# Kernel optimization log

Measured on AMD Instinct MI355X. Metric: run time of the kernel, lower is better.

The kernel has to match this reference:

```python
import jax, jax.numpy as jnp
import numpy as np

M = 8      # quantization steps
K = 256    # codewords per step
D = 128    # vector dim
H = 256    # hidden dim of residual MLP
S = M - 1  # number of neural steps (steps 1..M-1)
L = 2      # residual blocks per step
BEAM = 16  # beam width (cfg.B)
A = 8      # substep shortlist size (n_codes)
B = 2048   # batch


def setup_inputs() -> dict:
    key = jax.random.key(0)
    ks = jax.random.split(key, 16)
    sc = 0.05
    f32 = jnp.float32
    return {
        "x": jax.random.normal(ks[0], (B, D), f32),
        "codebook": jax.random.normal(ks[1], (M, K, D), f32) * sc,
        "codebook_rq": jax.random.normal(ks[2], (S, K, D), f32) * sc,
        "W_in": jax.random.normal(ks[3], (S, D, H), f32) * (D ** -0.5),
        "b_in": jnp.zeros((S, H), f32),
        "W_cat": jax.random.normal(ks[4], (S, H + D, H), f32) * ((H + D) ** -0.5),
        "b_cat": jnp.zeros((S, H), f32),
        "W1": jax.random.normal(ks[5], (S, L, H, H), f32) * (H ** -0.5),
        "b1": jnp.zeros((S, L, H), f32),
        "W2": jax.random.normal(ks[6], (S, L, H, H), f32) * (H ** -0.5),
        "b2": jnp.zeros((S, L, H), f32),
        "W_out": jax.random.normal(ks[7], (S, H, D), f32) * (H ** -0.5),
        "b_out": jnp.zeros((S, D), f32),
    }


def _approx_dist(q, cb):
    # approx squared L2 dist, dropping the query norm: ||c||^2 - 2 q.c
    # q: (..., D), cb: (K, D) -> (..., K)
    return jnp.sum(cb * cb, axis=-1) - 2.0 * q @ cb.T


def reference(x, codebook, codebook_rq, W_in, b_in, W_cat, b_cat,
              W1, b1, W2, b2, W_out, b_out):
    # --- step 0: plain codebook lookup, keep top-BEAM candidates ---
    d0 = _approx_dist(x, codebook[0])                  # (B, K)
    _, codes0 = jax.lax.top_k(-d0, BEAM)               # (B, BEAM) smallest dists
    xhat = codebook[0][codes0]                          # (B, BEAM, D)
    codes_list = [codes0]

    for s in range(S):
        i_step = s + 1
        F_in = xhat.shape[1]
        F_out = BEAM if i_step < M - 1 else 1

        # substep pre-filter: shortlist A codes per beam element
        xt = x[:, None, :] - xhat                      # (B, F, D)
        d = _approx_dist(xt, codebook_rq[s])           # (B, F, K)
        _, top_c = jax.lax.top_k(-d, A)                # (B, F, A)
        cw = codebook[i_step][top_c]                   # gather: (B, F, A, D)
        cw_res = cw

        # residual MLP conditioned on current xhat
        h = cw @ W_in[s] + b_in[s]                     # (B, F, A, H)
        xb = jnp.broadcast_to(xhat[:, :, None, :], cw.shape)
        h = jnp.concatenate([h, xb], axis=-1) @ W_cat[s] + b_cat[s]
        for l in range(L):
            h = h + jax.nn.relu(h @ W1[s, l] + b1[s, l]) @ W2[s, l] + b2[s, l]
        cw = h @ W_out[s] + b_out[s] + cw_res          # res_codeword_coeff = 1.0

        # re-score flattened beam*shortlist candidates and prune to F_out
        cand = (cw + xhat[:, :, None, :]).reshape(B, F_in * A, D)
        d2 = jnp.sum(cand * cand, axis=-1) - 2.0 * jnp.einsum('bd,bkd->bk', x, cand)
        _, idx = jax.lax.top_k(-d2, F_out)             # (B, F_out)

        parent = idx // A                               # == repeat_interleave+gather
        codes_list = [jnp.take_along_axis(c, parent, axis=-1) for c in codes_list]
        codes_list.append(jnp.take_along_axis(top_c.reshape(B, F_in * A), idx, axis=-1))
        xhat = jnp.take_along_axis(cand, idx[:, :, None], axis=1)  # (B, F_out, D)

    codes_MB = jnp.stack([c[:, 0] for c in codes_list])  # (M, B), final beam = 1
    return codes_MB, xhat[:, 0, :]
```

## Files before the change

### kernel.cpp

```cpp
#include <hip/hip_runtime.h>
#include <float.h>

#define BB    2048
#define DD    128
#define KK    256
#define HH    256
#define MM    8
#define SS    7
#define BEAMW 16
#define AA    8
#define WM    64

typedef _Float16 f16x8 __attribute__((ext_vector_type(8)));
typedef float    f32x4 __attribute__((ext_vector_type(4)));

#define HSWZ(row, m) (((row) << 5) + ((((m) + ((((row) >> 3)) << 2))) & 31))

__device__ __forceinline__ int hoff(int m, int j) {
  return m * 256 + ((((j >> 3) ^ (m & 7)) << 3) | (j & 7));
}

__global__ __launch_bounds__(64) void step0_kernel(
    const float* __restrict__ x, const float* __restrict__ cb,
    float* __restrict__ xhat, int* __restrict__ codes)
{
  int b = blockIdx.x, l = threadIdx.x;
  __shared__ float xs[DD];
  xs[l]      = x[b * DD + l];
  xs[l + 64] = x[b * DD + 64 + l];
  __syncthreads();
  float dist[4];
#pragma unroll
  for (int q = 0; q < 4; ++q) {
    const float* row = cb + (size_t)(q * 64 + l) * DD;
    float dot = 0.f, nrm = 0.f;
#pragma unroll 8
    for (int d = 0; d < DD; d += 4) {
      float4 c = *(const float4*)(row + d);
      dot += c.x * xs[d] + c.y * xs[d + 1] + c.z * xs[d + 2] + c.w * xs[d + 3];
      nrm += c.x * c.x + c.y * c.y + c.z * c.z + c.w * c.w;
    }
    dist[q] = nrm - 2.f * dot;
  }
  for (int it = 0; it < BEAMW; ++it) {
    float bv = dist[0]; int bi = l;
#pragma unroll
    for (int q = 1; q < 4; ++q) {
      if (dist[q] < bv) { bv = dist[q]; bi = q * 64 + l; }
    }
#pragma unroll
    for (int mmk = 1; mmk < 64; mmk <<= 1) {
      float ov = __shfl_xor(bv, mmk);
      int   oi = __shfl_xor(bi, mmk);
      if (ov < bv || (ov == bv && oi < bi)) { bv = ov; bi = oi; }
    }
    const float* crow = cb + (size_t)bi * DD;
    float2 v = *(const float2*)(crow + l * 2);
    *(float2*)(xhat + (size_t)(b * BEAMW + it) * DD + l * 2) = v;
    if (l == 0) codes[(b * BEAMW + it) * MM] = bi;
    if (l == (bi & 63)) dist[bi >> 6] = FLT_MAX;
  }
}

__global__ __launch_bounds__(128) void rqprep_kernel(
    const float* __restrict__ rq, float* __restrict__ rqT, float* __restrict__ rqn)
{
  int k = blockIdx.x, d = threadIdx.x;
  float v = rq[k * DD + d];
  rqT[d * KK + k] = v;
  float p = v * v;
#pragma unroll
  for (int mmk = 1; mmk < 64; mmk <<= 1) p += __shfl_xor(p, mmk);
  __shared__ float ps[2];
  if ((d & 63) == 0) ps[d >> 6] = p;
  __syncthreads();
  if (d == 0) rqn[k] = ps[0] + ps[1];
}

__global__ __launch_bounds__(256) void codeterm_kernel(
    const float* __restrict__ cbstep, const float* __restrict__ Win,
    const float* __restrict__ bin, const float* __restrict__ Wcat,
    const float* __restrict__ bcat, float* __restrict__ ct)
{
  int k = blockIdx.x, j = threadIdx.x;
  __shared__ float crow[DD];
  __shared__ float h1[HH];
  if (j < DD) crow[j] = cbstep[k * DD + j];
  __syncthreads();
  float a = bin[j];
  for (int d = 0; d < DD; ++d) a += crow[d] * Win[d * HH + j];
  h1[j] = a;
  __syncthreads();
  float c = bcat[j];
  for (int t = 0; t < HH; ++t) c += h1[t] * Wcat[t * HH + j];
  ct[k * HH + j] = c;
}

__global__ __launch_bounds__(256) void wpack_kernel(
    const float* __restrict__ W1s, const float* __restrict__ W2s,
    const float* __restrict__ Wouts, const float* __restrict__ Wcat2s,
    _Float16* __restrict__ wAh, _Float16* __restrict__ wAl,
    _Float16* __restrict__ woh, _Float16* __restrict__ wol,
    _Float16* __restrict__ wch, _Float16* __restrict__ wcl)
{
  int t = blockIdx.x * 256 + threadIdx.x;
  const float* src; _Float16 *dh, *dl;
  int N, r;
  if (t < 32768) {
    int mi = t >> 13; r = t & 8191;
    src = (mi & 1 ? W2s : W1s) + (size_t)(mi >> 1) * HH * HH;
    dh = wAh + (size_t)mi * 65536; dl = wAl + (size_t)mi * 65536;
    N = 256;
  } else if (t < 36864) {
    r = t - 32768; src = Wouts; dh = woh; dl = wol; N = 128;
  } else {
    r = t - 36864; src = Wcat2s; dh = wch; dl = wcl; N = 256;
  }
  int l = r & 63;
  int nct = N >> 4;
  int c = (r >> 6) & (nct - 1);
  int q = r / (64 * nct);
  int k0 = q * 32 + (l >> 4) * 8;
  int col = c * 16 + (l & 15);
  size_t fo = (size_t)r * 8;
#pragma unroll
  for (int j = 0; j < 8; ++j) {
    float v = src[(size_t)(k0 + j) * N + col];
    _Float16 hi = (_Float16)v;
    dh[fo + j] = hi;
    dl[fo + j] = (_Float16)((v - (float)hi) * 2048.0f);
  }
}

__global__ __launch_bounds__(256) void xterm_kernel(
    const float* __restrict__ xhat,
    const _Float16* __restrict__ wch, const _Float16* __restrict__ wcl,
    float* __restrict__ xtg)
{
  int tid = threadIdx.x;
  int l = tid & 63, w = tid >> 6;
  int lg = l >> 4, lr = l & 15;
  int r0 = blockIdx.x * 16;
  const f32x4 z4 = {0.f, 0.f, 0.f, 0.f};
  f32x4 a1[4], a2[4];
#pragma unroll
  for (int c = 0; c < 4; ++c) { a1[c] = z4; a2[c] = z4; }
  for (int q = 0; q < 4; ++q) {
    const float* ap = xhat + (size_t)(r0 + lr) * DD + q * 32 + lg * 8;
    float4 f0 = *(const float4*)ap;
    float4 f1 = *(const float4*)(ap + 4);
    float fv[8] = {f0.x, f0.y, f0.z, f0.w, f1.x, f1.y, f1.z, f1.w};
    f16x8 Ah, Al;
#pragma unroll
    for (int j = 0; j < 8; ++j) {
      _Float16 hi = (_Float16)fv[j];
      Ah[j] = hi;
      Al[j] = (_Float16)((fv[j] - (float)hi) * 2048.0f);
    }
#pragma unroll
    for (int c = 0; c < 4; ++c) {
      size_t boff = ((size_t)(q * 16 + w * 4 + c) * 64 + l) * 8;
      f16x8 Bh = *(const f16x8*)&wch[boff];
      f16x8 Bl = *(const f16x8*)&wcl[boff];
      a1[c] = __builtin_amdgcn_mfma_f32_16x16x32_f16(Ah, Bh, a1[c], 0, 0, 0);
      a2[c] = __builtin_amdgcn_mfma_f32_16x16x32_f16(Al, Bh, a2[c], 0, 0, 0);
      a2[c] = __builtin_amdgcn_mfma_f32_16x16x32_f16(Ah, Bl, a2[c], 0, 0, 0);
    }
  }
#pragma unroll
  for (int c = 0; c < 4; ++c) {
    int col = (w * 4 + c) * 16 + lr;
#pragma unroll
    for (int r = 0; r < 4; ++r) {
      int row = r0 + lg * 4 + r;
      xtg[(size_t)row * 256 + col] = a1[c][r] + a2[c][r] * (1.0f / 2048.0f);
    }
  }
}

__global__ __launch_bounds__(256) void prefilter_kernel(
    const float* __restrict__ x, const float* __restrict__ xhat,
    const float* __restrict__ rqT, const float* __restrict__ rqn,
    int* __restrict__ topc)
{
  __shared__ float xtT[DD * 32];
  __shared__ float distb[32 * KK];
  int tid = threadIdx.x;
  int bf0 = blockIdx.x * 32;
  for (int i = 0; i < 16; ++i) {
    int idx = tid + i * 256;
    int d = idx >> 5, r = idx & 31;
    int bf = bf0 + r;
    xtT[HSWZ(d, r)] = x[(bf >> 4) * DD + d] - xhat[(size_t)bf * DD + d];
  }
  __syncthreads();
  int jb = tid & 31, mb = tid >> 5;
  float acc[4][8];
#pragma unroll
  for (int i = 0; i < 4; ++i)
#pragma unroll
    for (int jj = 0; jj < 8; ++jj) acc[i][jj] = 0.f;
  for (int d = 0; d < DD; ++d) {
    float4 hv = *(float4*)&xtT[HSWZ(d, mb * 4)];
    float4 w0 = *(const float4*)&rqT[d * KK + jb * 8];
    float4 w1 = *(const float4*)&rqT[d * KK + jb * 8 + 4];
    float hvv[4] = {hv.x, hv.y, hv.z, hv.w};
    float wv[8]  = {w0.x, w0.y, w0.z, w0.w, w1.x, w1.y, w1.z, w1.w};
#pragma unroll
    for (int i = 0; i < 4; ++i)
#pragma unroll
      for (int jj = 0; jj < 8; ++jj) acc[i][jj] += hvv[i] * wv[jj];
  }
#pragma unroll
  for (int i = 0; i < 4; ++i) {
    int r = mb * 4 + i;
#pragma unroll
    for (int jj = 0; jj < 8; ++jj) {
      int k = jb * 8 + jj;
      distb[r * KK + k] = rqn[k] - 2.f * acc[i][jj];
    }
  }
  __syncthreads();
  int wv2 = tid >> 6, lane = tid & 63;
  for (int rr = 0; rr < 8; ++rr) {
    int r = wv2 * 8 + rr;
    float v[4];
#pragma unroll
    for (int q = 0; q < 4; ++q) v[q] = distb[r * KK + lane + q * 64];
    int bfr = bf0 + r;
    for (int it = 0; it < AA; ++it) {
      float bv = v[0]; int bi = lane;
#pragma unroll
      for (int q = 1; q < 4; ++q) {
        if (v[q] < bv) { bv = v[q]; bi = q * 64 + lane; }
      }
#pragma unroll
      for (int mmk = 1; mmk < 64; mmk <<= 1) {
        float ov = __shfl_xor(bv, mmk);
        int   oi = __shfl_xor(bi, mmk);
        if (ov < bv || (ov == bv && oi < bi)) { bv = ov; bi = oi; }
      }
      if (lane == (bi & 63)) v[bi >> 6] = FLT_MAX;
      if (lane == 0) topc[bfr * AA + it] = bi;
    }
  }
}

__global__ __launch_bounds__(1024, 4) void mlp_kernel(
    const float* __restrict__ x, const float* __restrict__ xhat,
    const int* __restrict__ topc, const float* __restrict__ ct,
    const float* __restrict__ cbstep, const float* __restrict__ xtg,
    const _Float16* __restrict__ wAh, const _Float16* __restrict__ wAl,
    const _Float16* __restrict__ woh, const _Float16* __restrict__ wol,
    const float* __restrict__ b1a, const float* __restrict__ b2a,
    const float* __restrict__ bout,
    float* __restrict__ cand, float* __restrict__ d2g)
{
  __shared__ _Float16 hhi[WM * 256], hlo[WM * 256];
  __shared__ float xs[DD];
  __shared__ float pd2[WM][8];
  __shared__ int   cl[WM];

  int tid = threadIdx.x;
  int l = tid & 63, w = tid >> 6;
  int lg = l >> 4, lr = l & 15;
  int bf0 = blockIdx.x * 8;
  int b = bf0 >> 4;
  const f32x4 z4 = {0.f, 0.f, 0.f, 0.f};

  if (tid < WM) cl[tid] = topc[bf0 * AA + tid];
  if (tid < DD) xs[tid] = x[b * DD + tid];
  __syncthreads();

  for (int i = 0; i < 16; ++i) {
    int e = tid + i * 1024;
    int m = e >> 8, j = e & 255;
    float v = ct[cl[m] * HH + j] + xtg[(size_t)(bf0 + (m >> 3)) * 256 + j];
    _Float16 hi = (_Float16)v;
    int off = hoff(m, j);
    hhi[off] = hi;
    hlo[off] = (_Float16)((v - (float)hi) * 2048.0f);
  }
  __syncthreads();

  int j0 = w * 16 + lr;

  for (int lay = 0; lay < 2; ++lay) {
    const _Float16* W1h = wAh + (size_t)(lay * 2 + 0) * 65536;
    const _Float16* W1l = wAl + (size_t)(lay * 2 + 0) * 65536;
    const _Float16* W2h = wAh + (size_t)(lay * 2 + 1) * 65536;
    const _Float16* W2l = wAl + (size_t)(lay * 2 + 1) * 65536;
    const float* bb1 = b1a + lay * HH;
    const float* bb2 = b2a + lay * HH;

    f32x4 a1[4], a2[4];
#pragma unroll
    for (int rt = 0; rt < 4; ++rt) { a1[rt] = z4; a2[rt] = z4; }
    for (int q = 0; q < 8; ++q) {
      size_t boff = ((size_t)(q * 16 + w) * 64 + l) * 8;
      f16x8 Bh = *(const f16x8*)&W1h[boff];
      f16x8 Bl = *(const f16x8*)&W1l[boff];
#pragma unroll
      for (int rt = 0; rt < 4; ++rt) {
        int arow = rt * 16 + lr;
        int aoff = arow * 256 + (((q * 4 + lg) ^ (arow & 7)) << 3);
        f16x8 Ah = *(f16x8*)&hhi[aoff];
        f16x8 Al = *(f16x8*)&hlo[aoff];
        a1[rt] = __builtin_amdgcn_mfma_f32_16x16x32_f16(Ah, Bh, a1[rt], 0, 0, 0);
        a2[rt] = __builtin_amdgcn_mfma_f32_16x16x32_f16(Al, Bh, a2[rt], 0, 0, 0);
        a2[rt] = __builtin_amdgcn_mfma_f32_16x16x32_f16(Ah, Bl, a2[rt], 0, 0, 0);
      }
    }
    {
      float bj = bb1[j0];
#pragma unroll
      for (int rt = 0; rt < 4; ++rt)
#pragma unroll
        for (int r = 0; r < 4; ++r) {
          int m = rt * 16 + lg * 4 + r;
          float u = fmaxf(a1[rt][r] + a2[rt][r] * (1.0f / 2048.0f) + bj, 0.f);
          int off = hoff(m, j0);
          float res = (float)hhi[off] + (float)hlo[off] * (1.0f / 2048.0f);
          a1[rt][r] = u;
          a2[rt][r] = res;
        }
    }
    __syncthreads();
#pragma unroll
    for (int rt = 0; rt < 4; ++rt)
#pragma unroll
      for (int r = 0; r < 4; ++r) {
        int m = rt * 16 + lg * 4 + r;
        float v = a1[rt][r];
        _Float16 hi = (_Float16)v;
        int off = hoff(m, j0);
        hhi[off] = hi;
        hlo[off] = (_Float16)((v - (float)hi) * 2048.0f);
      }
    __syncthreads();

#pragma unroll
    for (int rt = 0; rt < 4; ++rt) {
      a1[rt] = a2[rt];
      a2[rt] = z4;
    }
    for (int q = 0; q < 8; ++q) {
      size_t boff = ((size_t)(q * 16 + w) * 64 + l) * 8;
      f16x8 Bh = *(const f16x8*)&W2h[boff];
      f16x8 Bl = *(const f16x8*)&W2l[boff];
#pragma unroll
      for (int rt = 0; rt < 4; ++rt) {
        int arow = rt * 16 + lr;
        int aoff = arow * 256 + (((q * 4 + lg) ^ (arow & 7)) << 3);
        f16x8 Ah = *(f16x8*)&hhi[aoff];
        f16x8 Al = *(f16x8*)&hlo[aoff];
        a1[rt] = __builtin_amdgcn_mfma_f32_16x16x32_f16(Ah, Bh, a1[rt], 0, 0, 0);
        a2[rt] = __builtin_amdgcn_mfma_f32_16x16x32_f16(Al, Bh, a2[rt], 0, 0, 0);
        a2[rt] = __builtin_amdgcn_mfma_f32_16x16x32_f16(Ah, Bl, a2[rt], 0, 0, 0);
      }
    }
    {
      float bj = bb2[j0];
#pragma unroll
      for (int rt = 0; rt < 4; ++rt)
#pragma unroll
        for (int r = 0; r < 4; ++r)
          a1[rt][r] += a2[rt][r] * (1.0f / 2048.0f) + bj;
    }
    __syncthreads();
#pragma unroll
    for (int rt = 0; rt < 4; ++rt)
#pragma unroll
      for (int r = 0; r < 4; ++r) {
        int m = rt * 16 + lg * 4 + r;
        float v = a1[rt][r];
        _Float16 hi = (_Float16)v;
        int off = hoff(m, j0);
        hhi[off] = hi;
        hlo[off] = (_Float16)((v - (float)hi) * 2048.0f);
      }
    __syncthreads();
  }

  int c8 = w & 7, mh = w >> 3;
  f32x4 o1[2], o2[2];
  o1[0] = z4; o1[1] = z4; o2[0] = z4; o2[1] = z4;
  for (int q = 0; q < 8; ++q) {
    size_t boff = ((size_t)(q * 8 + c8) * 64 + l) * 8;
    f16x8 Bh = *(const f16x8*)&woh[boff];
    f16x8 Bl = *(const f16x8*)&wol[boff];
#pragma unroll
    for (int rr = 0; rr < 2; ++rr) {
      int arow = (mh * 2 + rr) * 16 + lr;
      int aoff = arow * 256 + (((q * 4 + lg) ^ (arow & 7)) << 3);
      f16x8 Ah = *(f16x8*)&hhi[aoff];
      f16x8 Al = *(f16x8*)&hlo[aoff];
      o1[rr] = __builtin_amdgcn_mfma_f32_16x16x32_f16(Ah, Bh, o1[rr], 0, 0, 0);
      o2[rr] = __builtin_amdgcn_mfma_f32_16x16x32_f16(Al, Bh, o2[rr], 0, 0, 0);
      o2[rr] = __builtin_amdgcn_mfma_f32_16x16x32_f16(Ah, Bl, o2[rr], 0, 0, 0);
    }
  }
  int ci0 = (blockIdx.x & 1) * WM;
  int d = c8 * 16 + lr;
  float bo = bout[d];
  float xsd = xs[d];
#pragma unroll
  for (int rr = 0; rr < 2; ++rr) {
    int rt = mh * 2 + rr;
    float p[4];
#pragma unroll
    for (int r = 0; r < 4; ++r) {
      int m = rt * 16 + lg * 4 + r;
      float v = o1[rr][r] + o2[rr][r] * (1.0f / 2048.0f) + bo
              + cbstep[(size_t)cl[m] * DD + d]
              + xhat[(size_t)(bf0 + (m >> 3)) * DD + d];
      cand[((size_t)(b * 128 + ci0 + m)) * DD + d] = v;
      p[r] = v * (v - 2.f * xsd);
    }
#pragma unroll
    for (int mk = 1; mk < 16; mk <<= 1) {
#pragma unroll
      for (int r = 0; r < 4; ++r) p[r] += __shfl_xor(p[r], mk);
    }
    if (lr == 0) {
#pragma unroll
      for (int r = 0; r < 4; ++r) pd2[rt * 16 + lg * 4 + r][c8] = p[r];
    }
  }
  __syncthreads();
  if (tid < WM) {
    float s = 0.f;
#pragma unroll
    for (int ww = 0; ww < 8; ++ww) s += pd2[tid][ww];
    d2g[b * 128 + ci0 + tid] = s;
  }
}

__global__ __launch_bounds__(64) void topk_update_kernel(
    const float* __restrict__ d2g, const float* __restrict__ cand,
    const int* __restrict__ codes_in, const int* __restrict__ topc,
    float* __restrict__ xhat_out, int* __restrict__ codes_out,
    int fout, int spos)
{
  int b = blockIdx.x, lane = threadIdx.x;
  float v0 = d2g[b * 128 + lane];
  float v1 = d2g[b * 128 + 64 + lane];
  for (int r = 0; r < fout; ++r) {
    float bv = v0; int bi = lane;
    if (v1 < bv) { bv = v1; bi = 64 + lane; }
#pragma unroll
    for (int mmk = 1; mmk < 64; mmk <<= 1) {
      float ov = __shfl_xor(bv, mmk);
      int   oi = __shfl_xor(bi, mmk);
      if (ov < bv || (ov == bv && oi < bi)) { bv = ov; bi = oi; }
    }
    int parent = bi >> 3, a = bi & 7;
    if (lane < MM) {
      int valc = (lane == spos) ? topc[(b * BEAMW + parent) * AA + a]
                                : codes_in[(b * BEAMW + parent) * MM + lane];
      codes_out[(b * BEAMW + r) * MM + lane] = valc;
    }
    const float* src = cand + ((size_t)(b * 128 + bi)) * DD;
    float2 t = *(const float2*)(src + lane * 2);
    *(float2*)(xhat_out + (size_t)(b * BEAMW + r) * DD + lane * 2) = t;
    if (bi < 64) { if (lane == bi) v0 = FLT_MAX; }
    else         { if (lane == bi - 64) v1 = FLT_MAX; }
  }
}

__global__ __launch_bounds__(64) void finalize_kernel(
    const int* __restrict__ codes_fin, const float* __restrict__ xhat_fin,
    float* __restrict__ out)
{
  int b = blockIdx.x, lane = threadIdx.x;
  float2 t = *(const float2*)(xhat_fin + (size_t)(b * BEAMW) * DD + lane * 2);
  *(float2*)(out + (size_t)MM * BB + (size_t)b * DD + lane * 2) = t;
  if (lane < MM) out[lane * BB + b] = (float)codes_fin[(b * BEAMW) * MM + lane];
}

extern "C" void kernel_launch(void* const* d_in, const int* in_sizes, int n_in,
                              void* d_out, int out_size, void* d_ws, size_t ws_size,
                              hipStream_t stream)
{
  (void)in_sizes; (void)n_in; (void)out_size; (void)ws_size;
  const float* x    = (const float*)d_in[0];
  const float* cb   = (const float*)d_in[1];
  const float* rq   = (const float*)d_in[2];
  const float* Win  = (const float*)d_in[3];
  const float* bin  = (const float*)d_in[4];
  const float* Wcat = (const float*)d_in[5];
  const float* bcat = (const float*)d_in[6];
  const float* W1   = (const float*)d_in[7];
  const float* b1   = (const float*)d_in[8];
  const float* W2   = (const float*)d_in[9];
  const float* b2   = (const float*)d_in[10];
  const float* Wout = (const float*)d_in[11];
  const float* bout = (const float*)d_in[12];
  float* out = (float*)d_out;

  char* ws = (char*)d_ws;
  size_t off = 0;
  auto alloc = [&](size_t bytes) -> void* {
    void* p = ws + off;
    off += (bytes + 255) & ~(size_t)255;
    return p;
  };
  float* X0    = (float*)alloc((size_t)BB * BEAMW * DD * 4);
  float* X1    = (float*)alloc((size_t)BB * BEAMW * DD * 4);
  int*   C0    = (int*)  alloc((size_t)BB * BEAMW * MM * 4);
  int*   C1    = (int*)  alloc((size_t)BB * BEAMW * MM * 4);
  int*   tc    = (int*)  alloc((size_t)BB * BEAMW * AA * 4);
  float* rqT   = (float*)alloc((size_t)DD * KK * 4);
  float* rqn   = (float*)alloc((size_t)KK * 4);
  float* ct    = (float*)alloc((size_t)KK * HH * 4);
  float* d2b   = (float*)alloc((size_t)BB * 128 * 4);
  float* candb = (float*)alloc((size_t)BB * 128 * DD * 4);
  float* xtg   = (float*)alloc((size_t)BB * BEAMW * 256 * 4);
  _Float16* wAh = (_Float16*)alloc((size_t)4 * 65536 * 2);
  _Float16* wAl = (_Float16*)alloc((size_t)4 * 65536 * 2);
  _Float16* woh = (_Float16*)alloc((size_t)32768 * 2);
  _Float16* wol = (_Float16*)alloc((size_t)32768 * 2);
  _Float16* wch = (_Float16*)alloc((size_t)32768 * 2);
  _Float16* wcl = (_Float16*)alloc((size_t)32768 * 2);

  step0_kernel<<<BB, 64, 0, stream>>>(x, cb, X0, C0);
  float* Xc = X0; float* Xn = X1;
  int* Cc = C0; int* Cn = C1;
  for (int s = 0; s < SS; ++s) {
    wpack_kernel<<<160, 256, 0, stream>>>(
        W1 + (size_t)s * 2 * HH * HH, W2 + (size_t)s * 2 * HH * HH,
        Wout + (size_t)s * HH * DD,
        Wcat + (size_t)s * 384 * HH + (size_t)256 * HH,
        wAh, wAl, woh, wol, wch, wcl);
    rqprep_kernel<<<KK, DD, 0, stream>>>(rq + (size_t)s * KK * DD, rqT, rqn);
    codeterm_kernel<<<KK, HH, 0, stream>>>(cb + (size_t)(s + 1) * KK * DD,
        Win + (size_t)s * DD * HH, bin + (size_t)s * HH,
        Wcat + (size_t)s * 384 * HH, bcat + (size_t)s * HH, ct);
    prefilter_kernel<<<(BB * BEAMW) / 32, 256, 0, stream>>>(x, Xc, rqT, rqn, tc);
    xterm_kernel<<<(BB * BEAMW) / 16, 256, 0, stream>>>(Xc, wch, wcl, xtg);
    mlp_kernel<<<(BB * BEAMW * AA) / WM, 1024, 0, stream>>>(x, Xc, tc, ct,
        cb + (size_t)(s + 1) * KK * DD, xtg,
        wAh, wAl, woh, wol,
        b1 + (size_t)s * 2 * HH, b2 + (size_t)s * 2 * HH,
        bout + (size_t)s * DD,
        candb, d2b);
    int fo = (s < SS - 1) ? BEAMW : 1;
    topk_update_kernel<<<BB, 64, 0, stream>>>(d2b, candb, Cc, tc, Xn, Cn, fo, s + 1);
    { float* t = Xc; Xc = Xn; Xn = t; }
    { int* t = Cc; Cc = Cn; Cn = t; }
  }
  finalize_kernel<<<BB, 64, 0, stream>>>(Cc, Xc, out);
}
```

Baseline: 4.654 ms.

## Batch per-step weight prep into single launches and keep MLP residual in registers

Weight packing, rq transpose/norm and codeword-term precomputation for all seven steps now run once, up front, in three launches writing per-step buffers, replacing 21 small launches inside the step loop. In the MLP kernel, the residual stream is kept in fp32 registers and the ReLU intermediate goes to separate LDS buffers (uhi/ulo). This drops one barrier plus a full LDS rewrite per half-layer and the hi/lo residual reconstruction. The cost is doubled LDS for the activation tiles (about 128KB per block), which may limit occupancy or fail to fit, plus larger workspace buffers.

```diff
diff --git a/kernel.cpp b/kernel.cpp
--- a/kernel.cpp
+++ b/kernel.cpp
@@ -63,58 +63,70 @@
 }
 
 __global__ __launch_bounds__(128) void rqprep_kernel(
-    const float* __restrict__ rq, float* __restrict__ rqT, float* __restrict__ rqn)
-{
-  int k = blockIdx.x, d = threadIdx.x;
-  float v = rq[k * DD + d];
-  rqT[d * KK + k] = v;
+    const float* __restrict__ rq, float* __restrict__ rqT7, float* __restrict__ rqn7)
+{
+  int s = blockIdx.x >> 8, k = blockIdx.x & 255, d = threadIdx.x;
+  float v = rq[(size_t)s * KK * DD + k * DD + d];
+  rqT7[(size_t)s * DD * KK + d * KK + k] = v;
   float p = v * v;
 #pragma unroll
   for (int mmk = 1; mmk < 64; mmk <<= 1) p += __shfl_xor(p, mmk);
   __shared__ float ps[2];
   if ((d & 63) == 0) ps[d >> 6] = p;
   __syncthreads();
-  if (d == 0) rqn[k] = ps[0] + ps[1];
+  if (d == 0) rqn7[s * KK + k] = ps[0] + ps[1];
 }
 
 __global__ __launch_bounds__(256) void codeterm_kernel(
-    const float* __restrict__ cbstep, const float* __restrict__ Win,
+    const float* __restrict__ cb, const float* __restrict__ Win,
     const float* __restrict__ bin, const float* __restrict__ Wcat,
-    const float* __restrict__ bcat, float* __restrict__ ct)
-{
-  int k = blockIdx.x, j = threadIdx.x;
+    const float* __restrict__ bcat, float* __restrict__ ct7)
+{
+  int s = blockIdx.x >> 8, k = blockIdx.x & 255, j = threadIdx.x;
+  const float* cbstep = cb + (size_t)(s + 1) * KK * DD;
+  const float* WinS   = Win + (size_t)s * DD * HH;
+  const float* WcatS  = Wcat + (size_t)s * 384 * HH;
   __shared__ float crow[DD];
   __shared__ float h1[HH];
   if (j < DD) crow[j] = cbstep[k * DD + j];
   __syncthreads();
-  float a = bin[j];
-  for (int d = 0; d < DD; ++d) a += crow[d] * Win[d * HH + j];
+  float a = bin[s * HH + j];
+  for (int d = 0; d < DD; ++d) a += crow[d] * WinS[d * HH + j];
   h1[j] = a;
   __syncthreads();
-  float c = bcat[j];
-  for (int t = 0; t < HH; ++t) c += h1[t] * Wcat[t * HH + j];
-  ct[k * HH + j] = c;
+  float c = bcat[s * HH + j];
+  for (int t = 0; t < HH; ++t) c += h1[t] * WcatS[t * HH + j];
+  ct7[(size_t)s * KK * HH + k * HH + j] = c;
 }
 
 __global__ __launch_bounds__(256) void wpack_kernel(
-    const float* __restrict__ W1s, const float* __restrict__ W2s,
-    const float* __restrict__ Wouts, const float* __restrict__ Wcat2s,
-    _Float16* __restrict__ wAh, _Float16* __restrict__ wAl,
-    _Float16* __restrict__ woh, _Float16* __restrict__ wol,
-    _Float16* __restrict__ wch, _Float16* __restrict__ wcl)
-{
-  int t = blockIdx.x * 256 + threadIdx.x;
+    const float* __restrict__ W1, const float* __restrict__ W2,
+    const float* __restrict__ Wout, const float* __restrict__ Wcat,
+    _Float16* __restrict__ wAh7, _Float16* __restrict__ wAl7,
+    _Float16* __restrict__ woh7, _Float16* __restrict__ wol7,
+    _Float16* __restrict__ wch7, _Float16* __restrict__ wcl7)
+{
+  int tg = blockIdx.x * 256 + threadIdx.x;
+  int s = tg / 40960;
+  int t = tg % 40960;
   const float* src; _Float16 *dh, *dl;
   int N, r;
   if (t < 32768) {
     int mi = t >> 13; r = t & 8191;
-    src = (mi & 1 ? W2s : W1s) + (size_t)(mi >> 1) * HH * HH;
-    dh = wAh + (size_t)mi * 65536; dl = wAl + (size_t)mi * 65536;
+    src = (mi & 1 ? W2 : W1) + (size_t)s * 2 * HH * HH + (size_t)(mi >> 1) * HH * HH;
+    dh = wAh7 + (size_t)s * 262144 + (size_t)mi * 65536;
+    dl = wAl7 + (size_t)s * 262144 + (size_t)mi * 65536;
     N = 256;
   } else if (t < 36864) {
-    r = t - 32768; src = Wouts; dh = woh; dl = wol; N = 128;
+    r = t - 32768;
+    src = Wout + (size_t)s * HH * DD;
+    dh = woh7 + (size_t)s * 32768; dl = wol7 + (size_t)s * 32768;
+    N = 128;
   } else {
-    r = t - 36864; src = Wcat2s; dh = wch; dl = wcl; N = 256;
+    r = t - 36864;
+    src = Wcat + (size_t)s * 384 * HH + (size_t)256 * HH;
+    dh = wch7 + (size_t)s * 32768; dl = wcl7 + (size_t)s * 32768;
+    N = 256;
   }
   int l = r & 63;
   int nct = N >> 4;
@@ -257,6 +269,7 @@
     float* __restrict__ cand, float* __restrict__ d2g)
 {
   __shared__ _Float16 hhi[WM * 256], hlo[WM * 256];
+  __shared__ _Float16 uhi[WM * 256], ulo[WM * 256];
   __shared__ float xs[DD];
   __shared__ float pd2[WM][8];
   __shared__ int   cl[WM];
@@ -272,26 +285,28 @@
   if (tid < DD) xs[tid] = x[b * DD + tid];
   __syncthreads();
 
-  for (int i = 0; i < 16; ++i) {
-    int e = tid + i * 1024;
-    int m = e >> 8, j = e & 255;
-    float v = ct[cl[m] * HH + j] + xtg[(size_t)(bf0 + (m >> 3)) * 256 + j];
-    _Float16 hi = (_Float16)v;
-    int off = hoff(m, j);
-    hhi[off] = hi;
-    hlo[off] = (_Float16)((v - (float)hi) * 2048.0f);
-  }
-  __syncthreads();
-
   int j0 = w * 16 + lr;
+
+  float hres[4][4];
+#pragma unroll
+  for (int rt = 0; rt < 4; ++rt)
+#pragma unroll
+    for (int r = 0; r < 4; ++r) {
+      int m = rt * 16 + lg * 4 + r;
+      float v = ct[cl[m] * HH + j0] + xtg[(size_t)(bf0 + (m >> 3)) * 256 + j0];
+      hres[rt][r] = v;
+      _Float16 hi = (_Float16)v;
+      int off = hoff(m, j0);
+      hhi[off] = hi;
+      hlo[off] = (_Float16)((v - (float)hi) * 2048.0f);
+    }
+  __syncthreads();
 
   for (int lay = 0; lay < 2; ++lay) {
     const _Float16* W1h = wAh + (size_t)(lay * 2 + 0) * 65536;
     const _Float16* W1l = wAl + (size_t)(lay * 2 + 0) * 65536;
     const _Float16* W2h = wAh + (size_t)(lay * 2 + 1) * 65536;
     const _Float16* W2l = wAl + (size_t)(lay * 2 + 1) * 65536;
-    const float* bb1 = b1a + lay * HH;
-    const float* bb2 = b2a + lay * HH;
 
     f32x4 a1[4], a2[4];
 #pragma unroll
@@ -312,36 +327,25 @@
       }
     }
     {
-      float bj = bb1[j0];
+      float bj = b1a[lay * HH + j0];
 #pragma unroll
       for (int rt = 0; rt < 4; ++rt)
 #pragma unroll
         for (int r = 0; r < 4; ++r) {
           int m = rt * 16 + lg * 4 + r;
           float u = fmaxf(a1[rt][r] + a2[rt][r] * (1.0f / 2048.0f) + bj, 0.f);
+          _Float16 hi = (_Float16)u;
           int off = hoff(m, j0);
-          float res = (float)hhi[off] + (float)hlo[off] * (1.0f / 2048.0f);
-          a1[rt][r] = u;
-          a2[rt][r] = res;
+          uhi[off] = hi;
+          ulo[off] = (_Float16)((u - (float)hi) * 2048.0f);
         }
     }
     __syncthreads();
-#pragma unroll
-    for (int rt = 0; rt < 4; ++rt)
-#pragma unroll
-      for (int r = 0; r < 4; ++r) {
-        int m = rt * 16 + lg * 4 + r;
-        float v = a1[rt][r];
-        _Float16 hi = (_Float16)v;
-        int off = hoff(m, j0);
-        hhi[off] = hi;
-        hlo[off] = (_Float16)((v - (float)hi) * 2048.0f);
-      }
-    __syncthreads();
 
 #pragma unroll
     for (int rt = 0; rt < 4; ++rt) {
-      a1[rt] = a2[rt];
+#pragma unroll
+      for (int r = 0; r < 4; ++r) a1[rt][r] = hres[rt][r];
       a2[rt] = z4;
     }
     for (int q = 0; q < 8; ++q) {
@@ -352,33 +356,28 @@
       for (int rt = 0; rt < 4; ++rt) {
         int arow = rt * 16 + lr;
         int aoff = arow * 256 + (((q * 4 + lg) ^ (arow & 7)) << 3);
-        f16x8 Ah = *(f16x8*)&hhi[aoff];
-        f16x8 Al = *(f16x8*)&hlo[aoff];
+        f16x8 Ah = *(f16x8*)&uhi[aoff];
+        f16x8 Al = *(f16x8*)&ulo[aoff];
         a1[rt] = __builtin_amdgcn_mfma_f32_16x16x32_f16(Ah, Bh, a1[rt], 0, 0, 0);
         a2[rt] = __builtin_amdgcn_mfma_f32_16x16x32_f16(Al, Bh, a2[rt], 0, 0, 0);
         a2[rt] = __builtin_amdgcn_mfma_f32_16x16x32_f16(Ah, Bl, a2[rt], 0, 0, 0);
       }
     }
     {
-      float bj = bb2[j0];
+      float bj = b2a[lay * HH + j0];
 #pragma unroll
       for (int rt = 0; rt < 4; ++rt)
 #pragma unroll
-        for (int r = 0; r < 4; ++r)
-          a1[rt][r] += a2[rt][r] * (1.0f / 2048.0f) + bj;
-    }
-    __syncthreads();
-#pragma unroll
-    for (int rt = 0; rt < 4; ++rt)
-#pragma unroll
-      for (int r = 0; r < 4; ++r) {
-        int m = rt * 16 + lg * 4 + r;
-        float v = a1[rt][r];
-        _Float16 hi = (_Float16)v;
-        int off = hoff(m, j0);
-        hhi[off] = hi;
-        hlo[off] = (_Float16)((v - (float)hi) * 2048.0f);
-      }
+        for (int r = 0; r < 4; ++r) {
+          int m = rt * 16 + lg * 4 + r;
+          float v = a1[rt][r] + a2[rt][r] * (1.0f / 2048.0f) + bj;
+          hres[rt][r] = v;
+          _Float16 hi = (_Float16)v;
+          int off = hoff(m, j0);
+          hhi[off] = hi;
+          hlo[off] = (_Float16)((v - (float)hi) * 2048.0f);
+        }
+    }
     __syncthreads();
   }
 
@@ -510,37 +509,37 @@
   int*   C0    = (int*)  alloc((size_t)BB * BEAMW * MM * 4);
   int*   C1    = (int*)  alloc((size_t)BB * BEAMW * MM * 4);
   int*   tc    = (int*)  alloc((size_t)BB * BEAMW * AA * 4);
-  float* rqT   = (float*)alloc((size_t)DD * KK * 4);
-  float* rqn   = (float*)alloc((size_t)KK * 4);
-  float* ct    = (float*)alloc((size_t)KK * HH * 4);
   float* d2b   = (float*)alloc((size_t)BB * 128 * 4);
   float* candb = (float*)alloc((size_t)BB * 128 * DD * 4);
   float* xtg   = (float*)alloc((size_t)BB * BEAMW * 256 * 4);
-  _Float16* wAh = (_Float16*)alloc((size_t)4 * 65536 * 2);
-  _Float16* wAl = (_Float16*)alloc((size_t)4 * 65536 * 2);
-  _Float16* woh = (_Float16*)alloc((size_t)32768 * 2);
-  _Float16* wol = (_Float16*)alloc((size_t)32768 * 2);
-  _Float16* wch = (_Float16*)alloc((size_t)32768 * 2);
-  _Float16* wcl = (_Float16*)alloc((size_t)32768 * 2);
+  float* rqT7  = (float*)alloc((size_t)SS * DD * KK * 4);
+  float* rqn7  = (float*)alloc((size_t)SS * KK * 4);
+  float* ct7   = (float*)alloc((size_t)SS * KK * HH * 4);
+  _Float16* wAh7 = (_Float16*)alloc((size_t)SS * 4 * 65536 * 2);
+  _Float16* wAl7 = (_Float16*)alloc((size_t)SS * 4 * 65536 * 2);
+  _Float16* woh7 = (_Float16*)alloc((size_t)SS * 32768 * 2);
+  _Float16* wol7 = (_Float16*)alloc((size_t)SS * 32768 * 2);
+  _Float16* wch7 = (_Float16*)alloc((size_t)SS * 32768 * 2);
+  _Float16* wcl7 = (_Float16*)alloc((size_t)SS * 32768 * 2);
+
+  wpack_kernel<<<(SS * 40960) / 256, 256, 0, stream>>>(
+      W1, W2, Wout, Wcat, wAh7, wAl7, woh7, wol7, wch7, wcl7);
+  rqprep_kernel<<<SS * KK, DD, 0, stream>>>(rq, rqT7, rqn7);
+  codeterm_kernel<<<SS * KK, HH, 0, stream>>>(cb, Win, bin, Wcat, bcat, ct7);
 
   step0_kernel<<<BB, 64, 0, stream>>>(x, cb, X0, C0);
   float* Xc = X0; float* Xn = X1;
   int* Cc = C0; int* Cn = C1;
   for (int s = 0; s < SS; ++s) {
-    wpack_kernel<<<160, 256, 0, stream>>>(
-        W1 + (size_t)s * 2 * HH * HH, W2 + (size_t)s * 2 * HH * HH,
-        Wout + (size_t)s * HH * DD,
-        Wcat + (size_t)s * 384 * HH + (size_t)256 * HH,
-        wAh, wAl, woh, wol, wch, wcl);
-    rqprep_kernel<<<KK, DD, 0, stream>>>(rq + (size_t)s * KK * DD, rqT, rqn);
-    codeterm_kernel<<<KK, HH, 0, stream>>>(cb + (size_t)(s + 1) * KK * DD,
-        Win + (size_t)s * DD * HH, bin + (size_t)s * HH,
-        Wcat + (size_t)s * 384 * HH, bcat + (size_t)s * HH, ct);
-    prefilter_kernel<<<(BB * BEAMW) / 32, 256, 0, stream>>>(x, Xc, rqT, rqn, tc);
-    xterm_kernel<<<(BB * BEAMW) / 16, 256, 0, stream>>>(Xc, wch, wcl, xtg);
-    mlp_kernel<<<(BB * BEAMW * AA) / WM, 1024, 0, stream>>>(x, Xc, tc, ct,
+    prefilter_kernel<<<(BB * BEAMW) / 32, 256, 0, stream>>>(
+        x, Xc, rqT7 + (size_t)s * DD * KK, rqn7 + (size_t)s * KK, tc);
+    xterm_kernel<<<(BB * BEAMW) / 16, 256, 0, stream>>>(
+        Xc, wch7 + (size_t)s * 32768, wcl7 + (size_t)s * 32768, xtg);
+    mlp_kernel<<<(BB * BEAMW * AA) / WM, 1024, 0, stream>>>(
+        x, Xc, tc, ct7 + (size_t)s * KK * HH,
         cb + (size_t)(s + 1) * KK * DD, xtg,
-        wAh, wAl, woh, wol,
+        wAh7 + (size_t)s * 262144, wAl7 + (size_t)s * 262144,
+        woh7 + (size_t)s * 32768, wol7 + (size_t)s * 32768,
         b1 + (size_t)s * 2 * HH, b2 + (size_t)s * 2 * HH,
         bout + (size_t)s * DD,
         candb, d2b);
```

Measured after the change: 6.016 ms. 29.3% more time.
